# Kernel optimization log

Hardware: AMD Instinct MI355X
Metric: run time of the kernel (lower is better)

Reference implementation:

```python
import jax, jax.numpy as jnp
import numpy as np

B, N, F_IN, F_OUT = 16, 128, 128, 128
E_OUT, B_IN, B_OUT = 16, 16, 16
CI, L1_OUT = 64, 256
NEG = -9e15


def _lstm_dir(x, Wih, Whh, bih, bhh, reverse=False):
    # x: [B, T, D]; torch gate order i, f, g, o
    Bx, T, _ = x.shape
    H = Whh.shape[1]
    xs = jnp.flip(x, 1) if reverse else x
    pre = xs @ Wih.T + bih + bhh  # [B, T, 4H]

    def step(carry, p):
        h, c = carry
        g = p + h @ Whh.T
        i, f, gg, o = jnp.split(g, 4, axis=-1)
        c = jax.nn.sigmoid(f) * c + jax.nn.sigmoid(i) * jnp.tanh(gg)
        h = jax.nn.sigmoid(o) * jnp.tanh(c)
        return (h, c), h

    h0 = jnp.zeros((Bx, H), x.dtype)
    _, hs = jax.lax.scan(step, (h0, h0), jnp.swapaxes(pre, 0, 1))
    hs = jnp.swapaxes(hs, 0, 1)  # [B, T, H]
    return jnp.flip(hs, 1) if reverse else hs


def setup_inputs() -> dict:
    key = jax.random.key(0)
    ks = jax.random.split(key, 20)
    s = 0.1
    inp = {
        "input": jax.random.normal(ks[0], (B, N, F_IN), jnp.float32),
        "adj": jax.random.randint(ks[1], (B, N, N), 0, 2).astype(jnp.int32),
        "weight": jax.random.normal(ks[2], (B, N, N, B_IN), jnp.float32),
        "W": jax.random.normal(ks[3], (F_IN, F_OUT), jnp.float32) * s,
        "a": jax.random.normal(ks[4], (2 * F_OUT, E_OUT), jnp.float32) * s,
        "W_wf": jax.random.normal(ks[5], (B_OUT, B_IN), jnp.float32) * s,
        "b_wf": jax.random.normal(ks[6], (B_OUT,), jnp.float32) * s,
        "W_fc": jax.random.normal(ks[7], (E_OUT + B_OUT,), jnp.float32) * s,
        "b_fc": jax.random.normal(ks[8], (), jnp.float32) * s,
        "W_fcc": jax.random.normal(ks[9], (F_OUT,), jnp.float32) * s,
        "b_fcc": jax.random.normal(ks[10], (), jnp.float32) * s,
        "W_out": jax.random.normal(ks[11], (L1_OUT, 2 * CI + F_OUT), jnp.float32) * s,
        "b_out": jax.random.normal(ks[12], (L1_OUT,), jnp.float32) * s,
        "Wih_f": jax.random.normal(ks[13], (4 * CI, N), jnp.float32) * s,
        "Whh_f": jax.random.normal(ks[14], (4 * CI, CI), jnp.float32) * s,
        "bih_f": jax.random.normal(ks[15], (4 * CI,), jnp.float32) * s,
        "bhh_f": jax.random.normal(ks[16], (4 * CI,), jnp.float32) * s,
        "Wih_b": jax.random.normal(ks[17], (4 * CI, N), jnp.float32) * s,
        "Whh_b": jax.random.normal(ks[18], (4 * CI, CI), jnp.float32) * s,
        "bih_b": jax.random.normal(ks[19], (4 * CI,), jnp.float32) * s,
        "bhh_b": jax.random.normal(jax.random.fold_in(key, 99), (4 * CI,), jnp.float32) * s,
    }
    return inp


def reference(input, adj, weight, W, a, W_wf, b_wf, W_fc, b_fc, W_fcc, b_fcc,
              W_out, b_out, Wih_f, Whh_f, bih_f, bhh_f, Wih_b, Whh_b, bih_b, bhh_b):
    h = input @ W  # [B, N, F_OUT]
    # faithful replication of torch repeat/cat/view (interleaved pairing)
    A = jnp.tile(h, (1, 1, N)).reshape(B, N * N, F_OUT)
    B2 = jnp.tile(h, (1, N, 1))  # [B, N*N, F]
    atom_trans = jnp.concatenate([A, B2], axis=1).reshape(B, N, N, 2 * F_OUT)
    e = atom_trans @ a  # [B, N, N, E_OUT]
    w = weight @ W_wf.T + b_wf  # [B, N, N, B_OUT]
    e = jax.nn.leaky_relu(jnp.concatenate([e, w], axis=3))
    e = jnp.einsum('bijd,d->bij', e, W_fc) + b_fc  # fc -> squeeze
    attention = jax.nn.softmax(jnp.where(adj > 0, e, NEG), axis=2)
    # dropout p=0 (eval) -> identity
    at_input = attention[..., None] * h[:, :, None, :]  # [B, N, N, F]
    hn = jax.nn.leaky_relu(jnp.einsum('bijf,f->bij', at_input, W_fcc) + b_fcc)
    hf = _lstm_dir(hn, Wih_f, Whh_f, bih_f, bhh_f, reverse=False)
    hb = _lstm_dir(hn, Wih_b, Whh_b, bih_b, bhh_b, reverse=True)
    hn = jax.nn.leaky_relu(jnp.concatenate([hf, hb], axis=-1))  # [B, N, 2*CI]
    h1 = jnp.einsum('bij,bjf->bif', attention, h)  # [B, N, F]
    h1 = jnp.concatenate([hn, h1], axis=2)  # [B, N, 2*CI+F]
    out = jnp.einsum('bnd,od->bno', h1, W_out) + b_out
    return jax.nn.elu(out)
```

## Files before the change

kernel.cpp:

```cpp
#include <hip/hip_runtime.h>
#include <math.h>

#define B 16
#define N 128
#define F 128
#define CI 64
#define NEG (-9e15f)

__device__ __forceinline__ float lrelu(float x){ return x > 0.f ? x : 0.01f*x; }
__device__ __forceinline__ float sigm(float x){ return 1.f/(1.f+expf(-x)); }

__global__ __launch_bounds__(128) void k1_h(const float* __restrict__ input,
        const float* __restrict__ W, const float* __restrict__ a,
        const float* __restrict__ W_fcc,
        float* __restrict__ h, float* __restrict__ ha1, float* __restrict__ ha2,
        float* __restrict__ hw) {
    int row = blockIdx.x;
    int t = threadIdx.x;
    __shared__ float x[F];
    __shared__ float hr[F];
    x[t] = input[row*F + t];
    __syncthreads();
    float acc = 0.f;
    #pragma unroll
    for (int k = 0; k < F; k++) acc += x[k] * W[k*F + t];
    h[row*F + t] = acc;
    hr[t] = acc;
    __syncthreads();
    if (t < 16) {
        float a1 = 0.f;
        #pragma unroll
        for (int f = 0; f < F; f++) a1 += hr[f] * a[f*16 + t];
        ha1[row*16 + t] = a1;
    } else if (t < 32) {
        int e = t - 16;
        float a2 = 0.f;
        #pragma unroll
        for (int f = 0; f < F; f++) a2 += hr[f] * a[(F+f)*16 + e];
        ha2[row*16 + e] = a2;
    } else if (t == 32) {
        float s = 0.f;
        #pragma unroll
        for (int f = 0; f < F; f++) s += hr[f] * W_fcc[f];
        hw[row] = s;
    }
}

__global__ __launch_bounds__(128) void k2_att(
        const float* __restrict__ ha1, const float* __restrict__ ha2,
        const float* __restrict__ weight, const int* __restrict__ adj,
        const float* __restrict__ W_wf, const float* __restrict__ b_wf,
        const float* __restrict__ W_fc, const float* __restrict__ b_fc,
        const float* __restrict__ b_fcc, const float* __restrict__ hw,
        const float* __restrict__ h,
        float* __restrict__ hn, float* __restrict__ h1) {
    int b  = blockIdx.x >> 4;
    int ic = blockIdx.x & 15;
    int j = threadIdx.x;
    int lane = j & 63, wid = j >> 6;
    __shared__ float att_lds[8][N];
    __shared__ float red[2];
    float bfc = b_fc[0], bfcc = b_fcc[0];
    #pragma unroll 1
    for (int ii = 0; ii < 8; ii++) {
        int i = ic*8 + ii;
        int r1, r2;
        if (i < 64) { r1 = 2*i + (j >= 64 ? 1 : 0); r2 = r1; }
        else        { r1 = (2*j) & 127; r2 = r1 + 1; }
        const float4* p1 = (const float4*)(ha1 + (b*N + r1)*16);
        const float4* p2 = (const float4*)(ha2 + (b*N + r2)*16);
        float e16[16];
        #pragma unroll
        for (int q = 0; q < 4; q++) {
            float4 v1 = p1[q], v2 = p2[q];
            e16[q*4+0]=v1.x+v2.x; e16[q*4+1]=v1.y+v2.y;
            e16[q*4+2]=v1.z+v2.z; e16[q*4+3]=v1.w+v2.w;
        }
        const float4* wv4 = (const float4*)(weight + ((size_t)((b*N+i)*N) + j)*16);
        float wvec[16];
        #pragma unroll
        for (int q = 0; q < 4; q++) {
            float4 v = wv4[q];
            wvec[q*4]=v.x; wvec[q*4+1]=v.y; wvec[q*4+2]=v.z; wvec[q*4+3]=v.w;
        }
        float val = bfc;
        #pragma unroll
        for (int e = 0; e < 16; e++) val += lrelu(e16[e]) * W_fc[e];
        #pragma unroll
        for (int o = 0; o < 16; o++) {
            float acc = b_wf[o];
            #pragma unroll
            for (int k = 0; k < 16; k++) acc += wvec[k] * W_wf[o*16 + k];
            val += lrelu(acc) * W_fc[16 + o];
        }
        int av = adj[(b*N+i)*N + j];
        float logit = av > 0 ? val : NEG;
        float m = logit;
        #pragma unroll
        for (int off = 32; off > 0; off >>= 1) m = fmaxf(m, __shfl_xor(m, off));
        if (lane == 0) red[wid] = m;
        __syncthreads();
        m = fmaxf(red[0], red[1]);
        __syncthreads();
        float ex = expf(logit - m);
        float s = ex;
        #pragma unroll
        for (int off = 32; off > 0; off >>= 1) s += __shfl_xor(s, off);
        if (lane == 0) red[wid] = s;
        __syncthreads();
        s = red[0] + red[1];
        __syncthreads();
        float att = ex / s;
        att_lds[ii][j] = att;
        hn[(b*N+i)*N + j] = lrelu(att * hw[b*N+i] + bfcc);
    }
    __syncthreads();
    float acc[8];
    #pragma unroll
    for (int ii = 0; ii < 8; ii++) acc[ii] = 0.f;
    for (int jj = 0; jj < N; jj++) {
        float hv = h[(b*N + jj)*F + j];
        #pragma unroll
        for (int ii = 0; ii < 8; ii++) acc[ii] += att_lds[ii][jj] * hv;
    }
    #pragma unroll
    for (int ii = 0; ii < 8; ii++) h1[(b*N + ic*8 + ii)*F + j] = acc[ii];
}

__global__ __launch_bounds__(256) void k4_pre(
        const float* __restrict__ hn,
        const float* __restrict__ Wih_f, const float* __restrict__ bih_f, const float* __restrict__ bhh_f,
        const float* __restrict__ Wih_b, const float* __restrict__ bih_b, const float* __restrict__ bhh_b,
        float* __restrict__ pre_f, float* __restrict__ pre_b) {
    int dir = blockIdx.y;
    int g = threadIdx.x;
    const float* Wih = dir ? Wih_b : Wih_f;
    float bias = dir ? (bih_b[g] + bhh_b[g]) : (bih_f[g] + bhh_f[g]);
    float* pre = dir ? pre_b : pre_f;
    int r0 = blockIdx.x * 16;
    __shared__ float hl[16][F];
    const float4* src = (const float4*)(hn + (size_t)r0*F);
    float4* dst = (float4*)(&hl[0][0]);
    dst[g] = src[g];
    dst[g+256] = src[g+256];
    __syncthreads();
    float acc[16];
    #pragma unroll
    for (int t = 0; t < 16; t++) acc[t] = bias;
    for (int jc = 0; jc < F; jc += 16) {
        float w[16];
        const float4* wp = (const float4*)(Wih + g*F + jc);
        #pragma unroll
        for (int q = 0; q < 4; q++) {
            float4 v = wp[q];
            w[q*4]=v.x; w[q*4+1]=v.y; w[q*4+2]=v.z; w[q*4+3]=v.w;
        }
        #pragma unroll
        for (int t = 0; t < 16; t++) {
            #pragma unroll
            for (int jj = 0; jj < 16; jj++) acc[t] += hl[t][jc+jj] * w[jj];
        }
    }
    #pragma unroll
    for (int t = 0; t < 16; t++) pre[(size_t)(r0+t)*256 + g] = acc[t];
}

__global__ __launch_bounds__(256) void k5_lstm(
        const float* __restrict__ pre_f, const float* __restrict__ pre_b,
        const float* __restrict__ Whh_f, const float* __restrict__ Whh_b,
        float* __restrict__ hf, float* __restrict__ hb) {
    int b = blockIdx.x;
    int dir = blockIdx.y;
    const float* pre = dir ? pre_b : pre_f;
    const float* Whh = dir ? Whh_b : Whh_f;
    float* hout = dir ? hb : hf;
    int g = threadIdx.x;
    float w[CI];
    const float4* wp = (const float4*)(Whh + g*CI);
    #pragma unroll
    for (int q = 0; q < CI/4; q++) {
        float4 v = wp[q];
        w[q*4]=v.x; w[q*4+1]=v.y; w[q*4+2]=v.z; w[q*4+3]=v.w;
    }
    __shared__ float h_l[CI];
    __shared__ float gate[256];
    if (g < CI) h_l[g] = 0.f;
    float c = 0.f;
    __syncthreads();
    int tt = dir ? (N-1) : 0;
    int step = dir ? -1 : 1;
    float pnext = pre[((size_t)b*N + tt)*256 + g];
    for (int t = 0; t < N; t++) {
        float acc = pnext;
        int tn = tt + step;
        if (t < N-1) pnext = pre[((size_t)b*N + tn)*256 + g];
        #pragma unroll
        for (int k = 0; k < CI; k++) acc += h_l[k] * w[k];
        gate[g] = acc;
        __syncthreads();
        if (g < CI) {
            float ig = gate[g], fg = gate[CI+g], gg = gate[2*CI+g], og = gate[3*CI+g];
            c = sigm(fg)*c + sigm(ig)*tanhf(gg);
            float hv = sigm(og)*tanhf(c);
            h_l[g] = hv;
            hout[((size_t)b*N + tt)*CI + g] = hv;
        }
        __syncthreads();
        tt = tn;
    }
}

__global__ __launch_bounds__(256) void k6_out(
        const float* __restrict__ hf, const float* __restrict__ hb,
        const float* __restrict__ h1, const float* __restrict__ W_out,
        const float* __restrict__ b_out, float* __restrict__ out) {
    int r0 = blockIdx.x * 8;
    int o = threadIdx.x;
    __shared__ float rl[8][256];
    #pragma unroll
    for (int rr = 0; rr < 8; rr++) {
        int row = r0 + rr;
        float v;
        if (o < 64)       v = lrelu(hf[row*CI + o]);
        else if (o < 128) v = lrelu(hb[row*CI + (o-64)]);
        else              v = h1[row*F + (o-128)];
        rl[rr][o] = v;
    }
    __syncthreads();
    float acc[8];
    float bo = b_out[o];
    #pragma unroll
    for (int rr = 0; rr < 8; rr++) acc[rr] = bo;
    for (int dc = 0; dc < 256; dc += 16) {
        float w[16];
        const float4* wp = (const float4*)(W_out + o*256 + dc);
        #pragma unroll
        for (int q = 0; q < 4; q++) {
            float4 v = wp[q];
            w[q*4]=v.x; w[q*4+1]=v.y; w[q*4+2]=v.z; w[q*4+3]=v.w;
        }
        #pragma unroll
        for (int rr = 0; rr < 8; rr++) {
            #pragma unroll
            for (int jj = 0; jj < 16; jj++) acc[rr] += rl[rr][dc+jj] * w[jj];
        }
    }
    #pragma unroll
    for (int rr = 0; rr < 8; rr++) {
        float x = acc[rr];
        out[(size_t)(r0+rr)*256 + o] = x > 0.f ? x : (expf(x) - 1.f);
    }
}

extern "C" void kernel_launch(void* const* d_in, const int* in_sizes, int n_in,
                              void* d_out, int out_size, void* d_ws, size_t ws_size,
                              hipStream_t stream) {
    const float* input = (const float*)d_in[0];
    const int*   adj   = (const int*)  d_in[1];
    const float* weight= (const float*)d_in[2];
    const float* W     = (const float*)d_in[3];
    const float* a     = (const float*)d_in[4];
    const float* W_wf  = (const float*)d_in[5];
    const float* b_wf  = (const float*)d_in[6];
    const float* W_fc  = (const float*)d_in[7];
    const float* b_fc  = (const float*)d_in[8];
    const float* W_fcc = (const float*)d_in[9];
    const float* b_fcc = (const float*)d_in[10];
    const float* W_out = (const float*)d_in[11];
    const float* b_out = (const float*)d_in[12];
    const float* Wih_f = (const float*)d_in[13];
    const float* Whh_f = (const float*)d_in[14];
    const float* bih_f = (const float*)d_in[15];
    const float* bhh_f = (const float*)d_in[16];
    const float* Wih_b = (const float*)d_in[17];
    const float* Whh_b = (const float*)d_in[18];
    const float* bih_b = (const float*)d_in[19];
    const float* bhh_b = (const float*)d_in[20];

    float* ws = (float*)d_ws;
    float* h    = ws;
    float* ha1  = ws + 262144;
    float* ha2  = ws + 294912;
    float* hw   = ws + 327680;
    float* hn   = ws + 329728;
    float* h1   = ws + 591872;
    float* pre_f= ws + 854016;
    float* pre_b= ws + 1378304;
    float* hf   = ws + 1902592;
    float* hb   = ws + 2033664;

    k1_h<<<B*N, 128, 0, stream>>>(input, W, a, W_fcc, h, ha1, ha2, hw);
    k2_att<<<B*16, 128, 0, stream>>>(ha1, ha2, weight, adj, W_wf, b_wf, W_fc,
                                     b_fc, b_fcc, hw, h, hn, h1);
    k4_pre<<<dim3(128, 2), 256, 0, stream>>>(hn, Wih_f, bih_f, bhh_f,
                                             Wih_b, bih_b, bhh_b, pre_f, pre_b);
    k5_lstm<<<dim3(B, 2), 256, 0, stream>>>(pre_f, pre_b, Whh_f, Whh_b, hf, hb);
    k6_out<<<256, 256, 0, stream>>>(hf, hb, h1, W_out, b_out, (float*)d_out);
}
```

Baseline: 278.4 us.

## Use register-broadcast LSTM recurrence, fast math, and more attention blocks

The LSTM kernel now keeps each hidden state in a register and broadcasts it across the wavefront with readlane instead of reading it from shared memory. It double-buffers the gate array so each timestep needs one barrier instead of two, and every wave computes the cell update redundantly. Sigmoid, tanh and exp switch to fast __expf and hardware reciprocal approximations. The attention kernel launches four times as many blocks, each handling 2 rows instead of 8, for more parallelism, at the cost of more repeated h reads in the aggregation step.

```diff
diff --git a/kernel.cpp b/kernel.cpp
--- a/kernel.cpp
+++ b/kernel.cpp
@@ -8,7 +8,12 @@
 #define NEG (-9e15f)
 
 __device__ __forceinline__ float lrelu(float x){ return x > 0.f ? x : 0.01f*x; }
-__device__ __forceinline__ float sigm(float x){ return 1.f/(1.f+expf(-x)); }
+__device__ __forceinline__ float fastrcp(float x){ return __builtin_amdgcn_rcpf(x); }
+__device__ __forceinline__ float sigm(float x){ return fastrcp(1.f + __expf(-x)); }
+__device__ __forceinline__ float tanh_f(float x){ return 1.f - 2.f*fastrcp(__expf(2.f*x) + 1.f); }
+__device__ __forceinline__ float rdlane(float v, int l) {
+    return __int_as_float(__builtin_amdgcn_readlane(__float_as_int(v), l));
+}
 
 __global__ __launch_bounds__(128) void k1_h(const float* __restrict__ input,
         const float* __restrict__ W, const float* __restrict__ a,
@@ -54,16 +59,16 @@
         const float* __restrict__ b_fcc, const float* __restrict__ hw,
         const float* __restrict__ h,
         float* __restrict__ hn, float* __restrict__ h1) {
-    int b  = blockIdx.x >> 4;
-    int ic = blockIdx.x & 15;
+    int b  = blockIdx.x >> 6;
+    int ic = blockIdx.x & 63;
     int j = threadIdx.x;
     int lane = j & 63, wid = j >> 6;
-    __shared__ float att_lds[8][N];
+    __shared__ float att_lds[2][N];
     __shared__ float red[2];
     float bfc = b_fc[0], bfcc = b_fcc[0];
     #pragma unroll 1
-    for (int ii = 0; ii < 8; ii++) {
-        int i = ic*8 + ii;
+    for (int ii = 0; ii < 2; ii++) {
+        int i = ic*2 + ii;
         int r1, r2;
         if (i < 64) { r1 = 2*i + (j >= 64 ? 1 : 0); r2 = r1; }
         else        { r1 = (2*j) & 127; r2 = r1 + 1; }
@@ -102,7 +107,7 @@
         __syncthreads();
         m = fmaxf(red[0], red[1]);
         __syncthreads();
-        float ex = expf(logit - m);
+        float ex = __expf(logit - m);
         float s = ex;
         #pragma unroll
         for (int off = 32; off > 0; off >>= 1) s += __shfl_xor(s, off);
@@ -115,16 +120,16 @@
         hn[(b*N+i)*N + j] = lrelu(att * hw[b*N+i] + bfcc);
     }
     __syncthreads();
-    float acc[8];
-    #pragma unroll
-    for (int ii = 0; ii < 8; ii++) acc[ii] = 0.f;
+    float acc[2];
+    #pragma unroll
+    for (int ii = 0; ii < 2; ii++) acc[ii] = 0.f;
     for (int jj = 0; jj < N; jj++) {
         float hv = h[(b*N + jj)*F + j];
         #pragma unroll
-        for (int ii = 0; ii < 8; ii++) acc[ii] += att_lds[ii][jj] * hv;
-    }
-    #pragma unroll
-    for (int ii = 0; ii < 8; ii++) h1[(b*N + ic*8 + ii)*F + j] = acc[ii];
+        for (int ii = 0; ii < 2; ii++) acc[ii] += att_lds[ii][jj] * hv;
+    }
+    #pragma unroll
+    for (int ii = 0; ii < 2; ii++) h1[(b*N + ic*2 + ii)*F + j] = acc[ii];
 }
 
 __global__ __launch_bounds__(256) void k4_pre(
@@ -175,6 +180,7 @@
     const float* Whh = dir ? Whh_b : Whh_f;
     float* hout = dir ? hb : hf;
     int g = threadIdx.x;
+    int lane = g & 63;
     float w[CI];
     const float4* wp = (const float4*)(Whh + g*CI);
     #pragma unroll
@@ -182,31 +188,35 @@
         float4 v = wp[q];
         w[q*4]=v.x; w[q*4+1]=v.y; w[q*4+2]=v.z; w[q*4+3]=v.w;
     }
-    __shared__ float h_l[CI];
-    __shared__ float gate[256];
-    if (g < CI) h_l[g] = 0.f;
+    __shared__ float gate[2][256];
+    float hreg = 0.f;
     float c = 0.f;
-    __syncthreads();
     int tt = dir ? (N-1) : 0;
     int step = dir ? -1 : 1;
     float pnext = pre[((size_t)b*N + tt)*256 + g];
+    int buf = 0;
     for (int t = 0; t < N; t++) {
-        float acc = pnext;
-        int tn = tt + step;
-        if (t < N-1) pnext = pre[((size_t)b*N + tn)*256 + g];
-        #pragma unroll
-        for (int k = 0; k < CI; k++) acc += h_l[k] * w[k];
-        gate[g] = acc;
-        __syncthreads();
-        if (g < CI) {
-            float ig = gate[g], fg = gate[CI+g], gg = gate[2*CI+g], og = gate[3*CI+g];
-            c = sigm(fg)*c + sigm(ig)*tanhf(gg);
-            float hv = sigm(og)*tanhf(c);
-            h_l[g] = hv;
-            hout[((size_t)b*N + tt)*CI + g] = hv;
-        }
-        __syncthreads();
-        tt = tn;
+        float a0 = pnext, a1 = 0.f, a2 = 0.f, a3 = 0.f;
+        if (t < N-1) pnext = pre[((size_t)b*N + tt + step)*256 + g];
+        #pragma unroll
+        for (int k = 0; k < CI; k += 4) {
+            a0 += rdlane(hreg, k+0) * w[k+0];
+            a1 += rdlane(hreg, k+1) * w[k+1];
+            a2 += rdlane(hreg, k+2) * w[k+2];
+            a3 += rdlane(hreg, k+3) * w[k+3];
+        }
+        gate[buf][g] = (a0 + a1) + (a2 + a3);
+        __syncthreads();
+        float ig = gate[buf][lane];
+        float fg = gate[buf][CI + lane];
+        float gg = gate[buf][2*CI + lane];
+        float og = gate[buf][3*CI + lane];
+        c = sigm(fg)*c + sigm(ig)*tanh_f(gg);
+        float hv = sigm(og)*tanh_f(c);
+        hreg = hv;
+        if (g < CI) hout[((size_t)b*N + tt)*CI + lane] = hv;
+        buf ^= 1;
+        tt += step;
     }
 }
 
@@ -248,7 +258,7 @@
     #pragma unroll
     for (int rr = 0; rr < 8; rr++) {
         float x = acc[rr];
-        out[(size_t)(r0+rr)*256 + o] = x > 0.f ? x : (expf(x) - 1.f);
+        out[(size_t)(r0+rr)*256 + o] = x > 0.f ? x : (__expf(x) - 1.f);
     }
 }
 
@@ -290,7 +300,7 @@
     float* hb   = ws + 2033664;
 
     k1_h<<<B*N, 128, 0, stream>>>(input, W, a, W_fcc, h, ha1, ha2, hw);
-    k2_att<<<B*16, 128, 0, stream>>>(ha1, ha2, weight, adj, W_wf, b_wf, W_fc,
+    k2_att<<<B*64, 128, 0, stream>>>(ha1, ha2, weight, adj, W_wf, b_wf, W_fc,
                                      b_fc, b_fcc, hw, h, hn, h1);
     k4_pre<<<dim3(128, 2), 256, 0, stream>>>(hn, Wih_f, bih_f, bhh_f,
                                              Wih_b, bih_b, bhh_b, pre_f, pre_b);
```

Measured after the change: 229.7 us. 17.5% less time.
